# Optimization experiments

Hardware: AMD Instinct MI355X
Metric: run time of the kernel (lower is better)

## Reference

```python
import jax, jax.numpy as jnp
import numpy as np

B_SZ, SEQ, CH, ORDER = 8, 8192, 256, 64
EPS_LN = 1e-5
EPS_H = 1e-6


def setup_inputs() -> dict:
    key = jax.random.key(0)
    ks = jax.random.split(key, 12)
    s = 1.0 / np.sqrt(CH)
    x = jax.random.normal(ks[0], (B_SZ, SEQ, CH), jnp.float32)
    # RTF params: A = denominator coeffs (monic, leading 1 implied), B = numerator coeffs
    A = 0.01 * jax.random.normal(ks[1], (CH, ORDER), jnp.float32)  # small -> stable 1/A(z)
    Bp = 0.1 * jax.random.normal(ks[2], (CH, ORDER), jnp.float32)
    h0 = jnp.zeros((1,), jnp.float32)  # init torch.tensor([0.])
    W_enc = s * jax.random.normal(ks[3], (CH, CH), jnp.float32)
    b_enc = jnp.zeros((CH,), jnp.float32)
    W_fc = s * jax.random.normal(ks[4], (CH, CH), jnp.float32)
    b_fc = jnp.zeros((CH,), jnp.float32)
    gamma = jnp.ones((CH,), jnp.float32)
    beta = jnp.zeros((CH,), jnp.float32)
    W_dec = s * jax.random.normal(ks[5], (CH, CH), jnp.float32)
    b_dec = jnp.zeros((CH,), jnp.float32)
    return {"x": x, "A": A, "Bp": Bp, "h0": h0, "W_enc": W_enc, "b_enc": b_enc,
            "W_fc": W_fc, "b_fc": b_fc, "gamma": gamma, "beta": beta,
            "W_dec": W_dec, "b_dec": b_dec}


def _rtf_kernel(A, Bp, L):
    # K(z) = B(z)/A(z) with monic denominator a = [1, A_1..A_order]
    C = A.shape[0]
    a = jnp.concatenate([jnp.ones((C, 1), A.dtype), A], axis=1)  # (C, order+1)
    af = jnp.fft.rfft(a, n=L, axis=1)
    bf = jnp.fft.rfft(Bp, n=L, axis=1)
    return jnp.fft.irfft(bf / af, n=L, axis=1)  # (C, L)


def _causal_fft_conv(x, K):
    # x: (B, L, C); K: (C, L) per-channel causal filter
    L = x.shape[1]
    n = 2 * L
    xf = jnp.fft.rfft(x, n=n, axis=1)            # (B, n/2+1, C)
    Kf = jnp.fft.rfft(K.T, n=n, axis=0)          # (n/2+1, C)
    return jnp.fft.irfft(xf * Kf[None], n=n, axis=1)[:, :L]


def reference(x, A, Bp, h0, W_enc, b_enc, W_fc, b_fc, gamma, beta, W_dec, b_dec):
    gelu = lambda t: jax.nn.gelu(t, approximate=False)
    xe = x @ W_enc.T + b_enc                      # encode
    L = xe.shape[1]
    K = _rtf_kernel(A, Bp, L)                     # kernel generation from (A,B)
    h1 = _causal_fft_conv(xe, K)                  # FFT long convolution
    y1 = gelu(h1 + h0 * xe)                       # SSMRTF output (mult_activation=gelu)
    y2 = gelu(y1 @ W_fc.T + b_fc)                 # fc + final_act
    y2 = y2 + xe                                  # skip
    mu = jnp.mean(y2, axis=-1, keepdims=True)     # LayerNorm over channels
    var = jnp.mean(jnp.square(y2 - mu), axis=-1, keepdims=True)
    y2 = (y2 - mu) * jax.lax.rsqrt(var + EPS_LN) * gamma + beta
    y = y2 @ W_dec.T + b_dec                      # decode
    # h = ||y||_inf over seq / ||x_enc||_inf over seq
    h = jnp.max(jnp.abs(y), axis=1) / (jnp.max(jnp.abs(xe), axis=1) + EPS_H)
    return (y, h)
```

## Files before the change

### kernel.cpp

```cpp
#include <hip/hip_runtime.h>
#include <math.h>


#define BSZ   8
#define SEQ   8192
#define CHN   256
#define ORD   64
#define STAPS 512
#define NDD   17
#define PREPAD 544
#define XROW  (PREPAD + SEQ)
#define MTOT  (BSZ * SEQ)
#define YELEMS (MTOT * CHN)

typedef short s16x8 __attribute__((ext_vector_type(8)));
typedef float f32x4 __attribute__((ext_vector_type(4)));

#define MFMA16(a, b, c) __builtin_amdgcn_mfma_f32_16x16x32_bf16((a), (b), (c), 0, 0, 0)

__device__ __forceinline__ void gll16(const void* g, void* l) {
  __builtin_amdgcn_global_load_lds(
      (const __attribute__((address_space(1))) unsigned int*)g,
      (__attribute__((address_space(3))) unsigned int*)l, 16, 0, 0);
}

#define PERMC(row, h) (((row) * 8 + ((h) ^ ((row) & 7))) * 8)

__device__ __forceinline__ unsigned short f2bf(float f) {
  unsigned u = __float_as_uint(f);
  return (unsigned short)((u + 0x7FFFu + ((u >> 16) & 1u)) >> 16);
}
__device__ __forceinline__ float bf2f(unsigned short h) {
  return __uint_as_float(((unsigned)h) << 16);
}
__device__ __forceinline__ float geluf(float x) {
  return 0.5f * x * (1.0f + erff(x * 0.70710678118654752f));
}
__device__ __forceinline__ uint4 packbf8(float4 a, float4 b) {
  uint4 r;
  r.x = (unsigned)f2bf(a.x) | ((unsigned)f2bf(a.y) << 16);
  r.y = (unsigned)f2bf(a.z) | ((unsigned)f2bf(a.w) << 16);
  r.z = (unsigned)f2bf(b.x) | ((unsigned)f2bf(b.y) << 16);
  r.w = (unsigned)f2bf(b.z) | ((unsigned)f2bf(b.w) << 16);
  return r;
}

__global__ __launch_bounds__(256) void k_prep(const float* we, const float* wf,
                                              const float* wd, unsigned short* owe,
                                              unsigned short* owf, unsigned short* owd) {
  int i = blockIdx.x * 256 + threadIdx.x;
  int which = i >> 16, off = i & 65535;
  if (which == 0)      owe[off] = f2bf(we[off]);
  else if (which == 1) owf[off] = f2bf(wf[off]);
  else                 owd[off] = f2bf(wd[off]);
}

__global__ __launch_bounds__(256) void k_zero(unsigned short* xeT, uint4* maxbufs) {
  int i = blockIdx.x * 256 + threadIdx.x;
  uint4 z; z.x = 0; z.y = 0; z.z = 0; z.w = 0;
  if (i < 2048 * 68) {
    int row = i / 68, cc = i % 68;
    *(uint4*)((char*)xeT + (size_t)row * (XROW * 2) + (size_t)cc * 16) = z;
  } else {
    int j = i - 2048 * 68;
    if (j < 1024) maxbufs[j] = z;
  }
}

__global__ __launch_bounds__(256) void k_kgen(const float* A, const float* Bp,
                                              unsigned short* afr) {
  __shared__ float Gs[4][STAPS];
  __shared__ float Et[4][64];
  __shared__ float Ac[4][65];
  __shared__ float Bb[4][64];
  __shared__ float Kb[4][STAPS];
  int lane = threadIdx.x & 63, wv = threadIdx.x >> 6;
  int c = blockIdx.x * 4 + wv;
  Ac[wv][lane + 1] = A[(size_t)c * ORD + lane];
  Bb[wv][lane]     = Bp[(size_t)c * ORD + lane];
  if (lane == 0) { Ac[wv][0] = 1.f; Gs[wv][0] = 1.f; }
  __syncthreads();

  for (int n = 1; n < STAPS; n <<= 1) {
    float e = 0.f;
    int uhi = min(n + lane, 64);
    for (int u = lane + 1; u <= uhi; ++u)
      e += Ac[wv][u] * Gs[wv][n + lane - u];
    Et[wv][lane] = e;
    __syncthreads();
    int nk = (n + 63) >> 6;
    for (int k = 0; k < nk; ++k) {
      int idx = k * 64 + lane;
      if (idx < n) {
        float acc = 0.f;
        int imax = min(idx, 63);
        for (int i = 0; i <= imax; ++i)
          acc += Et[wv][i] * Gs[wv][idx - i];
        Gs[wv][n + idx] = -acc;
      }
    }
    __syncthreads();
  }

  for (int k = 0; k < 8; ++k) {
    int t = k * 64 + lane;
    float acc = 0.f;
    int jmax = min(t, 63);
    for (int j = 0; j <= jmax; ++j)
      acc += Bb[wv][j] * Gs[wv][t - j];
    Kb[wv][t] = acc;
  }
  __syncthreads();

  int m = lane & 15, quad = lane >> 4;
  for (int dd = 0; dd < NDD; ++dd) {
    unsigned short v[8];
#pragma unroll
    for (int j = 0; j < 8; ++j) {
      int k = quad * 8 + j;
      int d = 2 * dd + (k >> 4);
      int p = k & 15;
      int s = 16 * d + m - p;
      float kv = (s >= 0 && s < STAPS) ? Kb[wv][s] : 0.f;
      v[j] = f2bf(kv);
    }
    uint4 pk;
    pk.x = (unsigned)v[0] | ((unsigned)v[1] << 16);
    pk.y = (unsigned)v[2] | ((unsigned)v[3] << 16);
    pk.z = (unsigned)v[4] | ((unsigned)v[5] << 16);
    pk.w = (unsigned)v[6] | ((unsigned)v[7] << 16);
    *(uint4*)(afr + ((size_t)(c * NDD + dd) * 64 + lane) * 8) = pk;
  }
}

__global__ __launch_bounds__(256) void k_gemm1(const float* x, const unsigned short* wb,
                                               const float* benc, unsigned short* xeT,
                                               unsigned int* maxxe) {
  __shared__ __align__(16) unsigned short As[256 * 64];
  __shared__ __align__(16) unsigned short Bs[64 * 64];
  int tid = threadIdx.x, lane = tid & 63, wv = tid >> 6;
  int ln15 = lane & 15, hf = lane >> 4;
  size_t t0 = (size_t)blockIdx.x * 64;
  int b = (int)(t0 >> 13), tin = (int)(t0 & 8191);
  f32x4 acc[4][4];
#pragma unroll
  for (int i = 0; i < 4; ++i)
#pragma unroll
    for (int j = 0; j < 4; ++j) { acc[i][j][0]=0.f; acc[i][j][1]=0.f; acc[i][j][2]=0.f; acc[i][j][3]=0.f; }

  for (int k0 = 0; k0 < CHN; k0 += 64) {
    __syncthreads();
#pragma unroll
    for (int i = 0; i < 8; ++i) {
      int p = 512 * wv + 64 * i + lane;
      int row = p >> 3, h = (p & 7) ^ (row & 7);
      gll16(wb + (size_t)row * CHN + k0 + h * 8, &As[(512 * wv + 64 * i) * 8]);
    }
    {
      int row = tid >> 2, hb = (tid & 3) * 2;
      const float* src = x + (t0 + row) * CHN + k0 + hb * 8;
      float4 f0 = *(const float4*)src;
      float4 f1 = *(const float4*)(src + 4);
      float4 f2 = *(const float4*)(src + 8);
      float4 f3 = *(const float4*)(src + 12);
      *(uint4*)&Bs[PERMC(row, hb)]     = packbf8(f0, f1);
      *(uint4*)&Bs[PERMC(row, hb + 1)] = packbf8(f2, f3);
    }
    __syncthreads();
#pragma unroll
    for (int ks = 0; ks < 2; ++ks) {
      s16x8 af[4], bfr[4];
#pragma unroll
      for (int mt = 0; mt < 4; ++mt) {
        int row = 64 * wv + 16 * mt + ln15;
        af[mt] = *(const s16x8*)&As[PERMC(row, ks * 4 + hf)];
      }
#pragma unroll
      for (int nt = 0; nt < 4; ++nt) {
        int row = 16 * nt + ln15;
        bfr[nt] = *(const s16x8*)&Bs[PERMC(row, ks * 4 + hf)];
      }
#pragma unroll
      for (int mt = 0; mt < 4; ++mt)
#pragma unroll
        for (int nt = 0; nt < 4; ++nt)
          acc[mt][nt] = MFMA16(af[mt], bfr[nt], acc[mt][nt]);
    }
  }
  int quad = hf;
#pragma unroll
  for (int mt = 0; mt < 4; ++mt) {
#pragma unroll
    for (int r = 0; r < 4; ++r) {
      int row = 64 * wv + 16 * mt + 4 * quad + r;
      float bias = benc[row];
      float mv = 0.f;
#pragma unroll
      for (int nt = 0; nt < 4; ++nt) {
        float v = acc[mt][nt][r] + bias;
        int t = tin + 16 * nt + ln15;
        xeT[(size_t)(b * CHN + row) * XROW + PREPAD + t] = f2bf(v);
        mv = fmaxf(mv, fabsf(v));
      }
      mv = fmaxf(mv, __shfl_xor(mv, 1)); mv = fmaxf(mv, __shfl_xor(mv, 2));
      mv = fmaxf(mv, __shfl_xor(mv, 4)); mv = fmaxf(mv, __shfl_xor(mv, 8));
      if (ln15 == 0) atomicMax(&maxxe[b * CHN + row], __float_as_uint(mv));
    }
  }
}

__global__ __launch_bounds__(256) void k_conv(const unsigned short* xeT,
                                              const unsigned short* afr,
                                              unsigned short* y1, const float* h0p) {
  __shared__ __align__(16) unsigned short xet[8 * 1024];
  __shared__ __align__(16) unsigned short bnc[8 * 256];
  int tid = threadIdx.x;
  int idx = blockIdx.x;
  int tg = idx & 31, cg = (idx >> 5) & 31, b = idx >> 10;
  int c0 = cg * 8, t0 = tg * 256;
  for (int i = tid; i < 800; i += 256) {
    int row = i / 100, cc = i % 100;
    uint4 v = *(const uint4*)(xeT + (size_t)(b * CHN + c0 + row) * XROW + t0 + cc * 8);
    int sw = cc ^ ((cc >> 3) & 7);
    *(uint4*)&xet[row * 1024 + sw * 8] = v;
  }
  __syncthreads();
  int lane = tid & 63, wv = tid >> 6;
  int n = lane & 15, quad = lane >> 4;
  int qc = quad - ((quad >> 1) << 2);
  float h0 = h0p[0];
#pragma unroll
  for (int ci = 0; ci < 2; ++ci) {
    int cl = wv * 2 + ci;
    int c = c0 + cl;
    f32x4 acc; acc[0]=0.f; acc[1]=0.f; acc[2]=0.f; acc[3]=0.f;
    const unsigned short* ap = afr + (size_t)c * (NDD * 512) + (size_t)lane * 8;
#pragma unroll 4
    for (int dd = 0; dd < NDD; ++dd) {
      s16x8 a = *(const s16x8*)(ap + (size_t)dd * 512);
      int cc = 2 * n - 4 * dd + 68 + qc;
      int sw = cc ^ ((cc >> 3) & 7);
      s16x8 bfr = *(const s16x8*)&xet[cl * 1024 + sw * 8];
      acc = MFMA16(a, bfr, acc);
    }
#pragma unroll
    for (int r = 0; r < 4; ++r) {
      int tl = 16 * n + 4 * quad + r;
      int e = PREPAD + tl;
      int ch = e >> 3, sw = ch ^ ((ch >> 3) & 7);
      float xv = bf2f(xet[cl * 1024 + sw * 8 + (e & 7)]);
      float v = acc[r] + h0 * xv;
      bnc[cl * 256 + tl] = f2bf(geluf(v));
    }
  }
  __syncthreads();
  {
    int tl = tid;
    uint4 pk;
    pk.x = (unsigned)bnc[0 * 256 + tl] | ((unsigned)bnc[1 * 256 + tl] << 16);
    pk.y = (unsigned)bnc[2 * 256 + tl] | ((unsigned)bnc[3 * 256 + tl] << 16);
    pk.z = (unsigned)bnc[4 * 256 + tl] | ((unsigned)bnc[5 * 256 + tl] << 16);
    pk.w = (unsigned)bnc[6 * 256 + tl] | ((unsigned)bnc[7 * 256 + tl] << 16);
    *(uint4*)(y1 + (size_t)(b * SEQ + t0 + tl) * CHN + c0) = pk;
  }
}

__global__ __launch_bounds__(256) void k_gemm2(const unsigned short* y1,
                                               const unsigned short* wb, const float* bfc,
                                               const unsigned short* xeT, const float* gam,
                                               const float* bet, unsigned short* y2n) {
  __shared__ __align__(16) unsigned short Ws[256 * 64];
  __shared__ __align__(16) unsigned short Asb[64 * 64];
  __shared__ float pl[64][2][2];
  int tid = threadIdx.x, lane = tid & 63, wv = tid >> 6;
  int ln15 = lane & 15, hf = lane >> 4, quad = hf;
  size_t M0 = (size_t)blockIdx.x * 64;
  int b = (int)(M0 >> 13), tin = (int)(M0 & 8191);
  int mh = wv & 1, nh = wv >> 1;
  f32x4 acc[2][8];
#pragma unroll
  for (int i = 0; i < 2; ++i)
#pragma unroll
    for (int j = 0; j < 8; ++j) { acc[i][j][0]=0.f; acc[i][j][1]=0.f; acc[i][j][2]=0.f; acc[i][j][3]=0.f; }

  for (int k0 = 0; k0 < CHN; k0 += 64) {
    __syncthreads();
#pragma unroll
    for (int i = 0; i < 8; ++i) {
      int p = 512 * wv + 64 * i + lane;
      int row = p >> 3, h = (p & 7) ^ (row & 7);
      gll16(wb + (size_t)row * CHN + k0 + h * 8, &Ws[(512 * wv + 64 * i) * 8]);
    }
#pragma unroll
    for (int i = 0; i < 2; ++i) {
      int p = 128 * wv + 64 * i + lane;
      int row = p >> 3, h = (p & 7) ^ (row & 7);
      gll16(y1 + (M0 + row) * CHN + k0 + h * 8, &Asb[(128 * wv + 64 * i) * 8]);
    }
    __syncthreads();
#pragma unroll
    for (int ks = 0; ks < 2; ++ks) {
      s16x8 af[2], bfr[8];
#pragma unroll
      for (int mt = 0; mt < 2; ++mt) {
        int row = 32 * mh + 16 * mt + ln15;
        af[mt] = *(const s16x8*)&Asb[PERMC(row, ks * 4 + hf)];
      }
#pragma unroll
      for (int nt = 0; nt < 8; ++nt) {
        int row = 128 * nh + 16 * nt + ln15;
        bfr[nt] = *(const s16x8*)&Ws[PERMC(row, ks * 4 + hf)];
      }
#pragma unroll
      for (int mt = 0; mt < 2; ++mt)
#pragma unroll
        for (int nt = 0; nt < 8; ++nt)
          acc[mt][nt] = MFMA16(af[mt], bfr[nt], acc[mt][nt]);
    }
  }
  float g8[8], be8[8], bf8[8];
#pragma unroll
  for (int nt = 0; nt < 8; ++nt) {
    int col = 128 * nh + 16 * nt + ln15;
    g8[nt] = gam[col]; be8[nt] = bet[col]; bf8[nt] = bfc[col];
  }
#pragma unroll
  for (int mt = 0; mt < 2; ++mt) {
    int mlb = 32 * mh + 16 * mt + 4 * quad;
    uint2 xv2[8];
#pragma unroll
    for (int nt = 0; nt < 8; ++nt) {
      int col = 128 * nh + 16 * nt + ln15;
      xv2[nt] = *(const uint2*)(xeT + (size_t)(b * CHN + col) * XROW + PREPAD + tin + mlb);
    }
#pragma unroll
    for (int r = 0; r < 4; ++r) {
      int ml = mlb + r;
      float s1 = 0.f, s2 = 0.f;
#pragma unroll
      for (int nt = 0; nt < 8; ++nt) {
        float t2 = acc[mt][nt][r] + bf8[nt];
        float xv = bf2f(((const unsigned short*)&xv2[nt])[r]);
        float y2 = geluf(t2) + xv;
        acc[mt][nt][r] = y2;
        s1 += y2; s2 += y2 * y2;
      }
      s1 += __shfl_xor(s1, 1); s2 += __shfl_xor(s2, 1);
      s1 += __shfl_xor(s1, 2); s2 += __shfl_xor(s2, 2);
      s1 += __shfl_xor(s1, 4); s2 += __shfl_xor(s2, 4);
      s1 += __shfl_xor(s1, 8); s2 += __shfl_xor(s2, 8);
      if (ln15 == 0) { pl[ml][nh][0] = s1; pl[ml][nh][1] = s2; }
    }
  }
  __syncthreads();
#pragma unroll
  for (int mt = 0; mt < 2; ++mt) {
#pragma unroll
    for (int r = 0; r < 4; ++r) {
      int ml = 32 * mh + 16 * mt + 4 * quad + r;
      float s1 = pl[ml][0][0] + pl[ml][1][0];
      float s2 = pl[ml][0][1] + pl[ml][1][1];
      float mu = s1 * (1.f / 256.f);
      float var = s2 * (1.f / 256.f) - mu * mu;
      float ri = rsqrtf(var + 1e-5f);
#pragma unroll
      for (int nt = 0; nt < 8; ++nt) {
        int col = 128 * nh + 16 * nt + ln15;
        float yn = (acc[mt][nt][r] - mu) * ri * g8[nt] + be8[nt];
        y2n[(M0 + ml) * CHN + col] = f2bf(yn);
      }
    }
  }
}

__global__ __launch_bounds__(256) void k_gemm3(const unsigned short* y2n,
                                               const unsigned short* wb, const float* bd,
                                               float* yout, unsigned int* maxy) {
  __shared__ __align__(16) unsigned short Ws[256 * 64];
  __shared__ __align__(16) unsigned short Asb[64 * 64];
  int tid = threadIdx.x, lane = tid & 63, wv = tid >> 6;
  int ln15 = lane & 15, hf = lane >> 4, quad = hf;
  size_t M0 = (size_t)blockIdx.x * 64;
  int b = (int)(M0 >> 13);
  int mh = wv & 1, nh = wv >> 1;
  f32x4 acc[2][8];
#pragma unroll
  for (int i = 0; i < 2; ++i)
#pragma unroll
    for (int j = 0; j < 8; ++j) { acc[i][j][0]=0.f; acc[i][j][1]=0.f; acc[i][j][2]=0.f; acc[i][j][3]=0.f; }

  for (int k0 = 0; k0 < CHN; k0 += 64) {
    __syncthreads();
#pragma unroll
    for (int i = 0; i < 8; ++i) {
      int p = 512 * wv + 64 * i + lane;
      int row = p >> 3, h = (p & 7) ^ (row & 7);
      gll16(wb + (size_t)row * CHN + k0 + h * 8, &Ws[(512 * wv + 64 * i) * 8]);
    }
#pragma unroll
    for (int i = 0; i < 2; ++i) {
      int p = 128 * wv + 64 * i + lane;
      int row = p >> 3, h = (p & 7) ^ (row & 7);
      gll16(y2n + (M0 + row) * CHN + k0 + h * 8, &Asb[(128 * wv + 64 * i) * 8]);
    }
    __syncthreads();
#pragma unroll
    for (int ks = 0; ks < 2; ++ks) {
      s16x8 af[2], bfr[8];
#pragma unroll
      for (int mt = 0; mt < 2; ++mt) {
        int row = 32 * mh + 16 * mt + ln15;
        af[mt] = *(const s16x8*)&Asb[PERMC(row, ks * 4 + hf)];
      }
#pragma unroll
      for (int nt = 0; nt < 8; ++nt) {
        int row = 128 * nh + 16 * nt + ln15;
        bfr[nt] = *(const s16x8*)&Ws[PERMC(row, ks * 4 + hf)];
      }
#pragma unroll
      for (int mt = 0; mt < 2; ++mt)
#pragma unroll
        for (int nt = 0; nt < 8; ++nt)
          acc[mt][nt] = MFMA16(af[mt], bfr[nt], acc[mt][nt]);
    }
  }
  float bd8[8];
#pragma unroll
  for (int nt = 0; nt < 8; ++nt) bd8[nt] = bd[128 * nh + 16 * nt + ln15];
#pragma unroll
  for (int mt = 0; mt < 2; ++mt)
#pragma unroll
    for (int r = 0; r < 4; ++r) {
      int ml = 32 * mh + 16 * mt + 4 * quad + r;
#pragma unroll
      for (int nt = 0; nt < 8; ++nt) {
        int col = 128 * nh + 16 * nt + ln15;
        float v = acc[mt][nt][r] + bd8[nt];
        acc[mt][nt][r] = v;
        yout[(M0 + ml) * CHN + col] = v;
      }
    }
#pragma unroll
  for (int nt = 0; nt < 8; ++nt) {
    int col = 128 * nh + 16 * nt + ln15;
    float mv = 0.f;
#pragma unroll
    for (int mt = 0; mt < 2; ++mt)
#pragma unroll
      for (int r = 0; r < 4; ++r) mv = fmaxf(mv, fabsf(acc[mt][nt][r]));
    mv = fmaxf(mv, __shfl_xor(mv, 16));
    mv = fmaxf(mv, __shfl_xor(mv, 32));
    if (quad == 0) atomicMax(&maxy[b * CHN + col], __float_as_uint(mv));
  }
}

__global__ __launch_bounds__(256) void k_hfin(const unsigned int* maxxe,
                                              const unsigned int* maxy, float* hout) {
  int i = blockIdx.x * 256 + threadIdx.x;
  if (i < BSZ * CHN) {
    float mx = __uint_as_float(maxxe[i]);
    float my = __uint_as_float(maxy[i]);
    hout[i] = my / (mx + 1e-6f);
  }
}

extern "C" void kernel_launch(void* const* d_in, const int* in_sizes, int n_in,
                              void* d_out, int out_size, void* d_ws, size_t ws_size,
                              hipStream_t stream) {
  const float* x   = (const float*)d_in[0];
  const float* A   = (const float*)d_in[1];
  const float* Bp  = (const float*)d_in[2];
  const float* h0  = (const float*)d_in[3];
  const float* We  = (const float*)d_in[4];
  const float* be  = (const float*)d_in[5];
  const float* Wf  = (const float*)d_in[6];
  const float* bfc = (const float*)d_in[7];
  const float* gam = (const float*)d_in[8];
  const float* bet = (const float*)d_in[9];
  const float* Wd  = (const float*)d_in[10];
  const float* bd  = (const float*)d_in[11];

  char* ws = (char*)d_ws;
  unsigned short* y1  = (unsigned short*)(ws + 0);
  unsigned short* afr = (unsigned short*)(ws + 33554432);
  unsigned short* web = (unsigned short*)(ws + 38010880);
  unsigned short* wfb = (unsigned short*)(ws + 38141952);
  unsigned short* wdb = (unsigned short*)(ws + 38273024);
  unsigned int*  maxxe = (unsigned int*)(ws + 38404096);
  unsigned int*  maxy  = (unsigned int*)(ws + 38412288);

  unsigned short* xeT = (unsigned short*)d_out;
  float* yout = (float*)d_out;
  float* hout = yout + YELEMS;

  k_prep<<<768, 256, 0, stream>>>(We, Wf, Wd, web, wfb, wdb);
  k_zero<<<548, 256, 0, stream>>>(xeT, (uint4*)maxxe);
  k_kgen<<<64, 256, 0, stream>>>(A, Bp, afr);
  k_gemm1<<<1024, 256, 0, stream>>>(x, web, be, xeT, maxxe);
  k_conv<<<8192, 256, 0, stream>>>(xeT, afr, y1, h0);
  k_gemm2<<<1024, 256, 0, stream>>>(y1, wfb, bfc, xeT, gam, bet, y1);
  k_gemm3<<<1024, 256, 0, stream>>>(y1, wdb, bd, yout, maxy);
  k_hfin<<<8, 256, 0, stream>>>(maxxe, maxy, hout);
}
```

Measured before the change: 325.8 us.

## Retile causal conv kernel with register-resident filter and longer time tiles

Each conv block now covers 4 channels by 2048 timesteps, one wave per channel, instead of 8 channels by 256 timesteps. The 17 filter fragments are loaded into registers once and reused across 8 sub-tiles. The input rows are fetched with direct global-to-LDS loads using a matching swizzle, and two accumulators split the MFMA dependency chain. This is meant to cut redundant halo loads and repeated filter fetches. The trade-off is that output stores become narrower 8-byte writes per row, and more registers are used per thread.

```diff
diff --git a/kernel.cpp b/kernel.cpp
--- a/kernel.cpp
+++ b/kernel.cpp
@@ -12,6 +12,9 @@
 #define XROW  (PREPAD + SEQ)
 #define MTOT  (BSZ * SEQ)
 #define YELEMS (MTOT * CHN)
+
+#define CT     2048
+#define CROWE  3072
 
 typedef short s16x8 __attribute__((ext_vector_type(8)));
 typedef float f32x4 __attribute__((ext_vector_type(4)));
@@ -212,56 +215,78 @@
 __global__ __launch_bounds__(256) void k_conv(const unsigned short* xeT,
                                               const unsigned short* afr,
                                               unsigned short* y1, const float* h0p) {
-  __shared__ __align__(16) unsigned short xet[8 * 1024];
-  __shared__ __align__(16) unsigned short bnc[8 * 256];
-  int tid = threadIdx.x;
+  __shared__ __align__(16) unsigned short xet[4 * CROWE];
+  __shared__ __align__(16) unsigned short bnc[4 * CT];
+  int tid = threadIdx.x, lane = tid & 63, wv = tid >> 6;
   int idx = blockIdx.x;
-  int tg = idx & 31, cg = (idx >> 5) & 31, b = idx >> 10;
-  int c0 = cg * 8, t0 = tg * 256;
-  for (int i = tid; i < 800; i += 256) {
-    int row = i / 100, cc = i % 100;
-    uint4 v = *(const uint4*)(xeT + (size_t)(b * CHN + c0 + row) * XROW + t0 + cc * 8);
-    int sw = cc ^ ((cc >> 3) & 7);
-    *(uint4*)&xet[row * 1024 + sw * 8] = v;
-  }
+  int tg = idx & 3, cg = (idx >> 2) & 63, b = idx >> 8;
+  int c0 = cg * 4, t0 = tg * CT;
+  int c = c0 + wv;
+
+  s16x8 afrg[NDD];
+  {
+    const unsigned short* ap = afr + (size_t)c * (NDD * 512) + (size_t)lane * 8;
+#pragma unroll
+    for (int dd = 0; dd < NDD; ++dd)
+      afrg[dd] = *(const s16x8*)(ap + (size_t)dd * 512);
+  }
+  {
+    int lp = lane ^ ((lane >> 3) & 7);
+    const unsigned short* gbase = xeT + (size_t)(b * CHN + c) * XROW + t0;
+    unsigned short* lbase = &xet[wv * CROWE];
+#pragma unroll
+    for (int k = 0; k < 6; ++k)
+      gll16(gbase + (size_t)(64 * k + lp) * 8, &lbase[k * 64 * 8]);
+  }
+  float h0 = h0p[0];
   __syncthreads();
-  int lane = tid & 63, wv = tid >> 6;
+
   int n = lane & 15, quad = lane >> 4;
   int qc = quad - ((quad >> 1) << 2);
-  float h0 = h0p[0];
-#pragma unroll
-  for (int ci = 0; ci < 2; ++ci) {
-    int cl = wv * 2 + ci;
-    int c = c0 + cl;
-    f32x4 acc; acc[0]=0.f; acc[1]=0.f; acc[2]=0.f; acc[3]=0.f;
-    const unsigned short* ap = afr + (size_t)c * (NDD * 512) + (size_t)lane * 8;
-#pragma unroll 4
-    for (int dd = 0; dd < NDD; ++dd) {
-      s16x8 a = *(const s16x8*)(ap + (size_t)dd * 512);
-      int cc = 2 * n - 4 * dd + 68 + qc;
-      int sw = cc ^ ((cc >> 3) & 7);
-      s16x8 bfr = *(const s16x8*)&xet[cl * 1024 + sw * 8];
-      acc = MFMA16(a, bfr, acc);
-    }
+  const unsigned short* xrow = &xet[wv * CROWE];
+#pragma unroll 1
+  for (int s = 0; s < 8; ++s) {
+    f32x4 a0, a1;
+    a0[0]=0.f; a0[1]=0.f; a0[2]=0.f; a0[3]=0.f;
+    a1[0]=0.f; a1[1]=0.f; a1[2]=0.f; a1[3]=0.f;
+    int cbase = 2 * n + qc + 68 + 32 * s;
+#pragma unroll
+    for (int dd = 0; dd < 16; dd += 2) {
+      int cc0 = cbase - 4 * dd, cc1 = cc0 - 4;
+      int sw0 = cc0 ^ ((cc0 >> 3) & 7), sw1 = cc1 ^ ((cc1 >> 3) & 7);
+      a0 = MFMA16(afrg[dd],     *(const s16x8*)&xrow[sw0 * 8], a0);
+      a1 = MFMA16(afrg[dd + 1], *(const s16x8*)&xrow[sw1 * 8], a1);
+    }
+    {
+      int cc = cbase - 64, sw = cc ^ ((cc >> 3) & 7);
+      a0 = MFMA16(afrg[16], *(const s16x8*)&xrow[sw * 8], a0);
+    }
+    unsigned short o[4];
 #pragma unroll
     for (int r = 0; r < 4; ++r) {
-      int tl = 16 * n + 4 * quad + r;
+      int tl = 256 * s + 16 * n + 4 * quad + r;
       int e = PREPAD + tl;
-      int ch = e >> 3, sw = ch ^ ((ch >> 3) & 7);
-      float xv = bf2f(xet[cl * 1024 + sw * 8 + (e & 7)]);
-      float v = acc[r] + h0 * xv;
-      bnc[cl * 256 + tl] = f2bf(geluf(v));
-    }
+      int ch = e >> 3, sw2 = ch ^ ((ch >> 3) & 7);
+      float xv = bf2f(xrow[sw2 * 8 + (e & 7)]);
+      float v = (a0[r] + a1[r]) + h0 * xv;
+      o[r] = f2bf(geluf(v));
+    }
+    uint2 pw;
+    pw.x = (unsigned)o[0] | ((unsigned)o[1] << 16);
+    pw.y = (unsigned)o[2] | ((unsigned)o[3] << 16);
+    *(uint2*)&bnc[wv * CT + 256 * s + 16 * n + 4 * quad] = pw;
   }
   __syncthreads();
   {
-    int tl = tid;
-    uint4 pk;
-    pk.x = (unsigned)bnc[0 * 256 + tl] | ((unsigned)bnc[1 * 256 + tl] << 16);
-    pk.y = (unsigned)bnc[2 * 256 + tl] | ((unsigned)bnc[3 * 256 + tl] << 16);
-    pk.z = (unsigned)bnc[4 * 256 + tl] | ((unsigned)bnc[5 * 256 + tl] << 16);
-    pk.w = (unsigned)bnc[6 * 256 + tl] | ((unsigned)bnc[7 * 256 + tl] << 16);
-    *(uint4*)(y1 + (size_t)(b * SEQ + t0 + tl) * CHN + c0) = pk;
+    const size_t obase = (size_t)(b * SEQ + t0) * CHN + c0;
+#pragma unroll
+    for (int s = 0; s < 8; ++s) {
+      int tl = 256 * s + tid;
+      uint2 pk;
+      pk.x = (unsigned)bnc[tl] | ((unsigned)bnc[CT + tl] << 16);
+      pk.y = (unsigned)bnc[2 * CT + tl] | ((unsigned)bnc[3 * CT + tl] << 16);
+      *(uint2*)(y1 + obase + (size_t)tl * CHN) = pk;
+    }
   }
 }
 
@@ -497,7 +522,7 @@
   k_zero<<<548, 256, 0, stream>>>(xeT, (uint4*)maxxe);
   k_kgen<<<64, 256, 0, stream>>>(A, Bp, afr);
   k_gemm1<<<1024, 256, 0, stream>>>(x, web, be, xeT, maxxe);
-  k_conv<<<8192, 256, 0, stream>>>(xeT, afr, y1, h0);
+  k_conv<<<2048, 256, 0, stream>>>(xeT, afr, y1, h0);
   k_gemm2<<<1024, 256, 0, stream>>>(y1, wfb, bfc, xeT, gam, bet, y1);
   k_gemm3<<<1024, 256, 0, stream>>>(y1, wdb, bd, yout, maxy);
   k_hfin<<<8, 256, 0, stream>>>(maxxe, maxy, hout);
```

Result: faster. 310.8 us (-4.6%).
